# Kernel tuning notes

Measured on AMD Instinct MI355X. Metric: run time of the kernel, lower is better.

## Reference

```python
import jax, jax.numpy as jnp
import numpy as np

VOCAB, EMBED, HID, SEQ, BATCH = 32000, 256, 512, 128, 256
U1, U2 = 256, 64


def setup_inputs() -> dict:
    key = jax.random.key(0)
    ks = jax.random.split(key, 8)
    s = 0.05  # small init scale keeps relu-LSTM states bounded
    return {
        "inputs": jax.random.randint(ks[0], (BATCH, SEQ), 0, VOCAB),
        "emb": jax.random.normal(ks[1], (VOCAB, EMBED), jnp.float32) * s,
        "W": jax.random.normal(ks[2], (EMBED, 4 * HID), jnp.float32) * s,
        "U": jax.random.normal(ks[3], (HID, 4 * HID), jnp.float32) * s,
        "b": jnp.zeros((4 * HID,), jnp.float32),
        "W2": jax.random.normal(ks[4], (HID, U1), jnp.float32) * s,
        "b2": jnp.zeros((U1,), jnp.float32),
        "W3": jax.random.normal(ks[5], (U1, U2), jnp.float32) * s,
        "b3": jnp.zeros((U2,), jnp.float32),
    }


def reference(inputs, emb, W, U, b, W2, b2, W3, b3):
    H = U.shape[0]
    x = emb[inputs]                      # [B, T, E] embedding lookup
    xW = jnp.einsum('bte,eg->btg', x, W) + b  # precompute input gate projections [B, T, 4H]

    def step(carry, xw_t):
        h, c = carry
        z = xw_t + h @ U                 # [B, 4H]; Keras gate order i, f, c, o
        i = jax.nn.sigmoid(z[:, :H])
        f = jax.nn.sigmoid(z[:, H:2 * H])
        g = jax.nn.relu(z[:, 2 * H:3 * H])   # activation='relu'
        o = jax.nn.sigmoid(z[:, 3 * H:])
        c = f * c + i * g
        h = o * jax.nn.relu(c)
        return (h, c), None

    B = x.shape[0]
    init = (jnp.zeros((B, H), x.dtype), jnp.zeros((B, H), x.dtype))
    (h, _), _ = jax.lax.scan(step, init, jnp.swapaxes(xW, 0, 1))  # scan over time

    y = jax.nn.relu(h @ W2 + b2)         # Dense head 1
    return jax.nn.softmax(y @ W3 + b3, axis=-1)  # Dense head 2 (softmax)
```

## Files before the change

### kernel.cpp

```cpp
#include <hip/hip_runtime.h>
#include <hip/hip_bf16.h>
#include <stdint.h>

#define B_  256
#define T_  128
#define E_  256
#define H_  512
#define G4  2048
#define U1_ 256
#define U2_ 64

#define HB_STEP   (16 * 16 * 64 * 8)
#define XF_STEP   (16 * 8 * 64 * 8)
#define SGN 0x8000800080008000ULL

typedef __attribute__((ext_vector_type(8))) short bf16x8;
typedef __attribute__((ext_vector_type(4))) float f32x4;
typedef __attribute__((ext_vector_type(2))) unsigned long long ullx2;
typedef unsigned long long ull;

static __device__ __forceinline__ unsigned short f2bf(float f) {
    unsigned u = __float_as_uint(f);
    unsigned r = (u + 0x7FFFu + ((u >> 16) & 1u)) >> 16;
    return (unsigned short)r;
}
static __device__ __forceinline__ ull ald(const ull* p) {
    return __hip_atomic_load(p, __ATOMIC_RELAXED, __HIP_MEMORY_SCOPE_AGENT);
}
static __device__ __forceinline__ void ast(ull* p, ull v) {
    __hip_atomic_store(p, v, __ATOMIC_RELAXED, __HIP_MEMORY_SCOPE_AGENT);
}

__global__ __launch_bounds__(256) void k_prep(const float* __restrict__ U,
                                              const float* __restrict__ W,
                                              short* __restrict__ wpk) {
    __shared__ float ld[32][64];
    const int bj = blockIdx.x;
    const int g  = bj >> 3;
    const int l0 = (bj & 7) * 64;
    const int t  = threadIdx.x;
    const int p   = t >> 4;
    const int hsl = p >> 1, blk = p & 1;
    const int ci  = t & 3;
    const int g4w = (t >> 2) & 3;
    const int hs  = (l0 >> 3) + hsl;
    const int c16 = g * 4 + ci;
    const int jloc = hsl * 8 + blk * 4 + ci;
    for (int kc = 0; kc < 24; ++kc) {
        const float* src = (kc < 16) ? (U + (long)(kc * 32) * G4)
                                     : (W + (long)((kc - 16) * 32) * G4);
        #pragma unroll
        for (int r = 0; r < 8; ++r) {
            int row = r * 4 + (t >> 6);
            ld[row][t & 63] = src[(long)row * G4 + g * 512 + l0 + (t & 63)];
        }
        __syncthreads();
        bf16x8 o;
        #pragma unroll
        for (int e = 0; e < 8; ++e) o[e] = (short)f2bf(ld[g4w * 8 + e][jloc]);
        *(bf16x8*)(wpk + (((long)(hs * 2 + blk) * 24 + kc) * 64 + (g4w * 16 + c16)) * 8) = o;
        __syncthreads();
    }
}

__global__ __launch_bounds__(256) void k_gather(const int* __restrict__ inp,
                                                const float* __restrict__ emb,
                                                short* __restrict__ xfrag) {
    const int tid  = threadIdx.x;
    const int wv   = tid >> 6;
    const int lane = tid & 63;
    const int c16  = lane & 15;
    const int g4   = lane >> 4;
    for (int it = 0; it < 16; ++it) {
        int task  = (it * 256 + blockIdx.x) * 4 + wv;
        int kc    = task & 7;
        int btile = (task >> 3) & 15;
        int t     = task >> 7;
        int b     = btile * 16 + c16;
        int idx   = inp[b * T_ + t];
        const float* src = emb + (long)idx * E_ + kc * 32 + g4 * 8;
        float4 v0 = *(const float4*)src;
        float4 v1 = *(const float4*)(src + 4);
        bf16x8 o;
        o[0]=(short)f2bf(v0.x); o[1]=(short)f2bf(v0.y); o[2]=(short)f2bf(v0.z); o[3]=(short)f2bf(v0.w);
        o[4]=(short)f2bf(v1.x); o[5]=(short)f2bf(v1.y); o[6]=(short)f2bf(v1.z); o[7]=(short)f2bf(v1.w);
        *(bf16x8*)(xfrag + ((long)((t * 16 + btile) * 8 + kc) * 64 + lane) * 8) = o;
    }
}

__global__ __launch_bounds__(256, 1) void k_lstm(
    const float* __restrict__ bias,
    const short* __restrict__ wpk,
    const short* __restrict__ xfrag,
    short* hfrag,
    float* hfin)
{
    __shared__ short lds[2][16][64][8];
    const int tid  = threadIdx.x;
    const int wid  = blockIdx.x;
    const int bt   = wid >> 4;
    const int hsg  = wid & 15;
    const int lane = tid & 63;
    const int wv   = tid >> 6;
    const int hs   = hsg * 4 + wv;
    const int c16  = lane & 15;
    const int g4   = lane >> 4;
    const int selfj = ((hsg >> 2) == wv) ? (hsg & 3) : -1;

    bf16x8 a_u[2][16], a_w[2][8];
    #pragma unroll
    for (int blk = 0; blk < 2; ++blk) {
        #pragma unroll
        for (int kc = 0; kc < 16; ++kc)
            a_u[blk][kc] = *(const bf16x8*)(wpk + (((long)(hs*2+blk)*24 + kc)*64 + lane)*8);
        #pragma unroll
        for (int kc = 0; kc < 8; ++kc)
            a_w[blk][kc] = *(const bf16x8*)(wpk + (((long)(hs*2+blk)*24 + 16 + kc)*64 + lane)*8);
    }
    float b0[4], b1[4];
    #pragma unroll
    for (int q = 0; q < 4; ++q) {
        b0[q] = bias[g4 * H_ + hs * 8 + q];
        b1[q] = bias[g4 * H_ + hs * 8 + 4 + q];
    }
    float cst[8];
    #pragma unroll
    for (int i = 0; i < 8; ++i) cst[i] = 0.f;

    ull* const pub0 = (ull*)hfrag + (((long)bt * 16 + hsg) * 64 + wv * 16 + c16) * 2;

    for (int t = 0; t < T_; ++t) {
        const int cb = t & 1;
        const ull* hp = (const ull*)hfrag + ((long)(t - 1) * HB_STEP) / 4;

        const short* xr = xfrag + (long)t * XF_STEP;
        bf16x8 xf[8];
        #pragma unroll
        for (int kc = 0; kc < 8; ++kc)
            xf[kc] = *(const bf16x8*)(xr + ((long)(bt * 8 + kc) * 64 + lane) * 8);

        ull LA[4], HA[4], LB[4], HB[4], L[4], Hh[4];
        if (t > 0) {
            #pragma unroll
            for (int j = 0; j < 4; ++j) if (j != selfj) {
                const ull* p = hp + (((long)bt * 16 + (wv * 4 + j)) * 64 + lane) * 2;
                LA[j] = ald(p); HA[j] = ald(p + 1);
            }
        }

        f32x4 a0 = (f32x4){b0[0], b0[1], b0[2], b0[3]};
        f32x4 a1 = (f32x4){b1[0], b1[1], b1[2], b1[3]};
        #pragma unroll
        for (int kc = 0; kc < 8; ++kc) {
            a0 = __builtin_amdgcn_mfma_f32_16x16x32_bf16(a_w[0][kc], xf[kc], a0, 0, 0, 0);
            a1 = __builtin_amdgcn_mfma_f32_16x16x32_bf16(a_w[1][kc], xf[kc], a1, 0, 0, 0);
        }

        if (t > 0) {
            unsigned stale = 0xFu & ~((selfj >= 0) ? (1u << selfj) : 0u);
            {
                unsigned ns = 0;
                #pragma unroll
                for (int j = 0; j < 4; ++j) if ((stale >> j) & 1u) {
                    if (__all(((LA[j] | HA[j]) & SGN) == 0)) { L[j] = LA[j]; Hh[j] = HA[j]; }
                    else ns |= (1u << j);
                }
                stale = ns;
            }
            if (stale) {
                #pragma unroll
                for (int j = 0; j < 4; ++j) if ((stale >> j) & 1u) {
                    const ull* p = hp + (((long)bt * 16 + (wv * 4 + j)) * 64 + lane) * 2;
                    LB[j] = ald(p); HB[j] = ald(p + 1);
                }
                for (int g = 0; g < (1 << 18); ++g) {
                    #pragma unroll
                    for (int j = 0; j < 4; ++j) if ((stale >> j) & 1u) {
                        const ull* p = hp + (((long)bt * 16 + (wv * 4 + j)) * 64 + lane) * 2;
                        LA[j] = ald(p); HA[j] = ald(p + 1);
                    }
                    unsigned ns = 0;
                    #pragma unroll
                    for (int j = 0; j < 4; ++j) if ((stale >> j) & 1u) {
                        if (__all(((LB[j] | HB[j]) & SGN) == 0)) { L[j] = LB[j]; Hh[j] = HB[j]; }
                        else ns |= (1u << j);
                    }
                    stale = ns;
                    if (!stale) break;
                    #pragma unroll
                    for (int j = 0; j < 4; ++j) if ((stale >> j) & 1u) {
                        const ull* p = hp + (((long)bt * 16 + (wv * 4 + j)) * 64 + lane) * 2;
                        LB[j] = ald(p); HB[j] = ald(p + 1);
                    }
                    ns = 0;
                    #pragma unroll
                    for (int j = 0; j < 4; ++j) if ((stale >> j) & 1u) {
                        if (__all(((LA[j] | HA[j]) & SGN) == 0)) { L[j] = LA[j]; Hh[j] = HA[j]; }
                        else ns |= (1u << j);
                    }
                    stale = ns;
                    if (!stale) break;
                }
            }
            #pragma unroll
            for (int j = 0; j < 4; ++j) if (j != selfj) {
                ullx2 u; u[0] = L[j]; u[1] = Hh[j];
                *(ullx2*)(&lds[cb][wv * 4 + j][lane][0]) = u;
            }
            #pragma unroll
            for (int kc = 0; kc < 16; ++kc) {
                if ((kc >> 2) != wv || (kc & 3) == selfj) continue;
                ullx2 u; u[0] = L[kc & 3]; u[1] = Hh[kc & 3];
                bf16x8 hf = __builtin_bit_cast(bf16x8, u);
                a0 = __builtin_amdgcn_mfma_f32_16x16x32_bf16(a_u[0][kc], hf, a0, 0, 0, 0);
                a1 = __builtin_amdgcn_mfma_f32_16x16x32_bf16(a_u[1][kc], hf, a1, 0, 0, 0);
            }
        }
        __syncthreads();

        if (t > 0) {
            #pragma unroll
            for (int kc = 0; kc < 16; ++kc) {
                if ((kc >> 2) == wv && (kc & 3) != selfj) continue;
                bf16x8 hf = *(const bf16x8*)(&lds[cb][kc][lane][0]);
                a0 = __builtin_amdgcn_mfma_f32_16x16x32_bf16(a_u[0][kc], hf, a0, 0, 0, 0);
                a1 = __builtin_amdgcn_mfma_f32_16x16x32_bf16(a_u[1][kc], hf, a1, 0, 0, 0);
            }
        }

        ull* const d = pub0 + (long)t * (HB_STEP / 4);
        float hv[8];
        #pragma unroll
        for (int q = 0; q < 4; ++q) {
            float z = a0[q];
            float a = (g4 == 2) ? fmaxf(z, 0.f) : 1.f / (1.f + __expf(-z));
            float ai = __shfl(a, c16,      64);
            float af = __shfl(a, c16 + 16, 64);
            float ag = __shfl(a, c16 + 32, 64);
            float ao = __shfl(a, c16 + 48, 64);
            float c_ = af * cst[q] + ai * ag;
            cst[q] = c_;
            hv[q] = ao * fmaxf(c_, 0.f);
        }
        ull p0 = (ull)f2bf(hv[0]) | ((ull)f2bf(hv[1])<<16)
               | ((ull)f2bf(hv[2])<<32) | ((ull)f2bf(hv[3])<<48);
        if (t < T_ - 1 && g4 == 0) ast(d, p0);
        #pragma unroll
        for (int q = 0; q < 4; ++q) {
            float z = a1[q];
            float a = (g4 == 2) ? fmaxf(z, 0.f) : 1.f / (1.f + __expf(-z));
            float ai = __shfl(a, c16,      64);
            float af = __shfl(a, c16 + 16, 64);
            float ag = __shfl(a, c16 + 32, 64);
            float ao = __shfl(a, c16 + 48, 64);
            float c_ = af * cst[4 + q] + ai * ag;
            cst[4 + q] = c_;
            hv[4 + q] = ao * fmaxf(c_, 0.f);
        }
        ull p1 = (ull)f2bf(hv[4]) | ((ull)f2bf(hv[5])<<16)
               | ((ull)f2bf(hv[6])<<32) | ((ull)f2bf(hv[7])<<48);

        if (t < T_ - 1) {
            if (g4 == 0) {
                ast(d + 1, p1);
                ullx2 u; u[0] = p0; u[1] = p1;
                *(ullx2*)(&lds[(t + 1) & 1][hsg][wv * 16 + c16][0]) = u;
            }
        } else {
            if (g4 == 0) {
                *(float4*)(hfin + ((long)bt * 16 + c16) * H_ + hs * 8)
                    = make_float4(hv[0], hv[1], hv[2], hv[3]);
                *(float4*)(hfin + ((long)bt * 16 + c16) * H_ + hs * 8 + 4)
                    = make_float4(hv[4], hv[5], hv[6], hv[7]);
            }
        }
    }
}

__global__ __launch_bounds__(256) void k_head(const float* __restrict__ hfin,
                                              const float* __restrict__ W2,
                                              const float* __restrict__ b2,
                                              const float* __restrict__ W3,
                                              const float* __restrict__ b3,
                                              float* __restrict__ out) {
    __shared__ float hs[H_];
    __shared__ float ys[U1_];
    __shared__ float ps[4][U2_];
    const int b = blockIdx.x, tid = threadIdx.x;
    if (tid < 128) *(float4*)(hs + tid * 4) = *(const float4*)(hfin + (long)b * H_ + tid * 4);
    __syncthreads();
    float acc = b2[tid];
    #pragma unroll 8
    for (int k = 0; k < H_; ++k) acc += hs[k] * W2[(long)k * U1_ + tid];
    ys[tid] = fmaxf(acc, 0.f);
    __syncthreads();
    const int u2 = tid & 63, part = tid >> 6;
    float p = 0.f;
    #pragma unroll 8
    for (int k = part * 64; k < part * 64 + 64; ++k) p += ys[k] * W3[(long)k * U2_ + u2];
    ps[part][u2] = p;
    __syncthreads();
    if (tid < 64) {
        float lg = b3[tid] + ps[0][tid] + ps[1][tid] + ps[2][tid] + ps[3][tid];
        float m = lg;
        #pragma unroll
        for (int off = 32; off >= 1; off >>= 1) m = fmaxf(m, __shfl_xor(m, off, 64));
        float e = __expf(lg - m);
        float s = e;
        #pragma unroll
        for (int off = 32; off >= 1; off >>= 1) s += __shfl_xor(s, off, 64);
        out[(long)b * U2_ + tid] = e / s;
    }
}

extern "C" void kernel_launch(void* const* d_in, const int* in_sizes, int n_in,
                              void* d_out, int out_size, void* d_ws, size_t ws_size,
                              hipStream_t stream) {
    const int*   inp = (const int*)d_in[0];
    const float* emb = (const float*)d_in[1];
    const float* W   = (const float*)d_in[2];
    const float* U   = (const float*)d_in[3];
    const float* bb  = (const float*)d_in[4];
    const float* W2  = (const float*)d_in[5];
    const float* b2  = (const float*)d_in[6];
    const float* W3  = (const float*)d_in[7];
    const float* b3  = (const float*)d_in[8];

    char* ws = (char*)d_ws;
    const long HB_BYTES = (long)(T_ - 1) * HB_STEP * 2;
    short* hfrag = (short*)ws;
    short* xfrag = (short*)(ws + HB_BYTES);
    short* wpk   = (short*)(ws + HB_BYTES + 16777216);
    float* hfin  = (float*)(ws + HB_BYTES + 16777216 + 3145728);

    hipMemsetAsync(hfrag, 0xAA, HB_BYTES, stream);
    k_prep<<<32, 256, 0, stream>>>(U, W, wpk);
    k_gather<<<256, 256, 0, stream>>>(inp, emb, xfrag);
    k_lstm<<<256, 256, 0, stream>>>(bb, wpk, xfrag, hfrag, hfin);
    k_head<<<B_, 256, 0, stream>>>(hfin, W2, b2, W3, b3, (float*)d_out);
}
```

Measured before the change: 507.6 us.

## Replace per-step hidden-state buffer with a 4-slot ring tagged by sign-bit parity

The recurrent hidden-state exchange buffer, which held a separate slot for every timestep, becomes a 4-slot ring. Readiness is now signalled by a parity bit in each bf16 sign bit that flips every four steps, and the consumer strips it before use. This is valid only because h is non-negative. The large per-call memset of the full-sequence buffer is replaced by a small fill kernel over a 1 MB ring, which should also keep the exchange traffic resident in cache. The cost is reliance on the sign-bit encoding and on the ring depth being enough that producers never overwrite a slot before slower peers have read it.

```diff
diff --git a/kernel.cpp b/kernel.cpp
--- a/kernel.cpp
+++ b/kernel.cpp
@@ -88,11 +88,16 @@
     }
 }
 
+__global__ __launch_bounds__(256) void k_fill(unsigned* __restrict__ p) {
+    int i = (blockIdx.x * 256 + threadIdx.x) * 4;
+    *(uint4*)(p + i) = make_uint4(0x00008000u, 0x00008000u, 0x00008000u, 0x00008000u);
+}
+
 __global__ __launch_bounds__(256, 1) void k_lstm(
     const float* __restrict__ bias,
     const short* __restrict__ wpk,
     const short* __restrict__ xfrag,
-    short* hfrag,
+    short* hring,
     float* hfin)
 {
     __shared__ short lds[2][16][64][8];
@@ -127,11 +132,12 @@
     #pragma unroll
     for (int i = 0; i < 8; ++i) cst[i] = 0.f;
 
-    ull* const pub0 = (ull*)hfrag + (((long)bt * 16 + hsg) * 64 + wv * 16 + c16) * 2;
+    ull* const pub0 = (ull*)hring + (((long)bt * 16 + hsg) * 64 + wv * 16 + c16) * 2;
 
     for (int t = 0; t < T_; ++t) {
         const int cb = t & 1;
-        const ull* hp = (const ull*)hfrag + ((long)(t - 1) * HB_STEP) / 4;
+        const ull* hp = (const ull*)hring + ((long)((t - 1) & 3) * HB_STEP) / 4;
+        const ull pm = (((t - 1) >> 2) & 1) ? SGN : 0ULL;
 
         const short* xr = xfrag + (long)t * XF_STEP;
         bf16x8 xf[8];
@@ -162,8 +168,9 @@
                 unsigned ns = 0;
                 #pragma unroll
                 for (int j = 0; j < 4; ++j) if ((stale >> j) & 1u) {
-                    if (__all(((LA[j] | HA[j]) & SGN) == 0)) { L[j] = LA[j]; Hh[j] = HA[j]; }
-                    else ns |= (1u << j);
+                    if (__all(((( LA[j] ^ pm) | (HA[j] ^ pm)) & SGN) == 0)) {
+                        L[j] = LA[j] & ~SGN; Hh[j] = HA[j] & ~SGN;
+                    } else ns |= (1u << j);
                 }
                 stale = ns;
             }
@@ -182,8 +189,9 @@
                     unsigned ns = 0;
                     #pragma unroll
                     for (int j = 0; j < 4; ++j) if ((stale >> j) & 1u) {
-                        if (__all(((LB[j] | HB[j]) & SGN) == 0)) { L[j] = LB[j]; Hh[j] = HB[j]; }
-                        else ns |= (1u << j);
+                        if (__all((((LB[j] ^ pm) | (HB[j] ^ pm)) & SGN) == 0)) {
+                            L[j] = LB[j] & ~SGN; Hh[j] = HB[j] & ~SGN;
+                        } else ns |= (1u << j);
                     }
                     stale = ns;
                     if (!stale) break;
@@ -195,8 +203,9 @@
                     ns = 0;
                     #pragma unroll
                     for (int j = 0; j < 4; ++j) if ((stale >> j) & 1u) {
-                        if (__all(((LA[j] | HA[j]) & SGN) == 0)) { L[j] = LA[j]; Hh[j] = HA[j]; }
-                        else ns |= (1u << j);
+                        if (__all((((LA[j] ^ pm) | (HA[j] ^ pm)) & SGN) == 0)) {
+                            L[j] = LA[j] & ~SGN; Hh[j] = HA[j] & ~SGN;
+                        } else ns |= (1u << j);
                     }
                     stale = ns;
                     if (!stale) break;
@@ -228,7 +237,8 @@
             }
         }
 
-        ull* const d = pub0 + (long)t * (HB_STEP / 4);
+        ull* const d = pub0 + (long)(t & 3) * (HB_STEP / 4);
+        const ull tw = ((t >> 2) & 1) ? SGN : 0ULL;
         float hv[8];
         #pragma unroll
         for (int q = 0; q < 4; ++q) {
@@ -244,7 +254,7 @@
         }
         ull p0 = (ull)f2bf(hv[0]) | ((ull)f2bf(hv[1])<<16)
                | ((ull)f2bf(hv[2])<<32) | ((ull)f2bf(hv[3])<<48);
-        if (t < T_ - 1 && g4 == 0) ast(d, p0);
+        if (t < T_ - 1 && g4 == 0) ast(d, p0 | tw);
         #pragma unroll
         for (int q = 0; q < 4; ++q) {
             float z = a1[q];
@@ -262,7 +272,7 @@
 
         if (t < T_ - 1) {
             if (g4 == 0) {
-                ast(d + 1, p1);
+                ast(d + 1, p1 | tw);
                 ullx2 u; u[0] = p0; u[1] = p1;
                 *(ullx2*)(&lds[(t + 1) & 1][hsg][wv * 16 + c16][0]) = u;
             }
@@ -327,15 +337,14 @@
     const float* b3  = (const float*)d_in[8];
 
     char* ws = (char*)d_ws;
-    const long HB_BYTES = (long)(T_ - 1) * HB_STEP * 2;
-    short* hfrag = (short*)ws;
-    short* xfrag = (short*)(ws + HB_BYTES);
-    short* wpk   = (short*)(ws + HB_BYTES + 16777216);
-    float* hfin  = (float*)(ws + HB_BYTES + 16777216 + 3145728);
-
-    hipMemsetAsync(hfrag, 0xAA, HB_BYTES, stream);
+    short* hring = (short*)ws;
+    short* xfrag = (short*)(ws + (1 << 20));
+    short* wpk   = (short*)(ws + (1 << 20) + 16777216);
+    float* hfin  = (float*)(ws + (1 << 20) + 16777216 + 3145728);
+
+    k_fill<<<256, 256, 0, stream>>>((unsigned*)hring);
     k_prep<<<32, 256, 0, stream>>>(U, W, wpk);
     k_gather<<<256, 256, 0, stream>>>(inp, emb, xfrag);
-    k_lstm<<<256, 256, 0, stream>>>(bb, wpk, xfrag, hfrag, hfin);
+    k_lstm<<<256, 256, 0, stream>>>(bb, wpk, xfrag, hring, hfin);
     k_head<<<B_, 256, 0, stream>>>(hfin, W2, b2, W3, b3, (float*)d_out);
 }
```

Result: slower. 518.6 us (+2.2%).
